# Performance work log

Measured on AMD Instinct MI355X. Metric: run time of the kernel, lower is better.

## Reference

```python
import jax, jax.numpy as jnp
import numpy as np

B, T, D = 2, 2048, 1024
H = 4            # num_heads (== num_kv_heads, num_kv_groups = 1)
W = 512          # window_size
S = 64           # state_size
CK = D // H      # head_k_dim = 256
CV = D // H      # head_v_dim = 256
EPS = 1e-5
SCALE = 1.0


def setup_inputs() -> dict:
    key = jax.random.key(0)
    ks = jax.random.split(key, 8)
    def w(k, o, i):
        return jax.random.normal(k, (o, i), jnp.float32) * 0.02
    return {
        "hidden_states": jax.random.normal(ks[0], (B, T, D), jnp.float32),
        "w_norm": jnp.ones((D,), jnp.float32),   # shared RMSNorm weight (pre- and post-norm; module overwrites self.norm)
        "Wq": w(ks[1], D, D),
        "Wk": w(ks[2], D, D),
        "Wv": w(ks[3], D, D),
        "Ws": w(ks[4], D, D),
        "Wg": w(ks[5], H * S, D),
        "Wo": w(ks[6], D, D),
    }


def _rms(x, w):
    return x * jax.lax.rsqrt(jnp.mean(x * x, axis=-1, keepdims=True) + EPS) * w


def reference(hidden_states, w_norm, Wq, Wk, Wv, Ws, Wg, Wo):
    h = _rms(hidden_states, w_norm)                           # pre-norm (norm_first)
    proj = lambda x, Wm: jnp.einsum('btd,od->bto', x, Wm)
    heads = lambda x, c: x.reshape(B, T, H, c).transpose(0, 2, 1, 3)
    q = heads(proj(h, Wq), CK) * SCALE                        # [B,H,T,CK]
    k = heads(proj(h, Wk), CK)
    v = heads(proj(h, Wv), CV)
    s = heads(proj(h, Ws), CK)                                # state-key projection
    g = jax.nn.softmax(proj(h, Wg), axis=-1)                  # softmax over full H*S dim (as in module)
    g = heads(g, S)                                           # [B,H,T,S] gate over state slots

    # ---- compressed global state (causal cumulative g-weighted outer products) ----
    # state_K[t] = sum_{t'<=t} g[t']^T s[t'];  scores_state[t,s] = q[t] . state_K[t,s]
    causal = jnp.tril(jnp.ones((T, T), dtype=bool))
    A = jnp.einsum('bhtc,bhuc->bhtu', q, s)                   # q . s per pair
    A = jnp.where(causal, A, 0.0)
    sc_state = jnp.einsum('bhtu,bhus->bhts', A, g)            # [B,H,T,S]

    # ---- sliding-window local attention (blocked: each query block sees prev+cur key block) ----
    nb = T // W
    qb = q.reshape(B, H, nb, W, CK)
    kb = k.reshape(B, H, nb, W, CK)
    vb = v.reshape(B, H, nb, W, CV)
    kprev = jnp.concatenate([jnp.zeros_like(kb[:, :, :1]), kb[:, :, :-1]], axis=2)
    vprev = jnp.concatenate([jnp.zeros_like(vb[:, :, :1]), vb[:, :, :-1]], axis=2)
    k2 = jnp.concatenate([kprev, kb], axis=3)                 # [B,H,nb,2W,CK]
    v2 = jnp.concatenate([vprev, vb], axis=3)                 # [B,H,nb,2W,CV]
    sc_w = jnp.einsum('bhnrc,bhnuc->bhnru', qb, k2)           # [B,H,nb,W,2W]

    r = jnp.arange(W)[:, None]
    u = jnp.arange(2 * W)[None, :]
    d = W + r - u                                             # distance t - t_key
    band = (d >= 0) & (d <= W - 1)                            # window of size W, causal
    first_blk = band & (u >= W)                               # block 0 has no real prev block
    wmask = jnp.where(jnp.arange(nb)[:, None, None] == 0, first_blk, band)   # [nb,W,2W]
    slopes = 2.0 ** (-8.0 * jnp.arange(H, dtype=jnp.float32) / H)            # [H]
    bias = -slopes[:, None, None] * d                          # alibi: slopes*(j-W+1) == -slope*dist
    sc_w = sc_w + bias[None, :, None, :, :]
    sc_w = jnp.where(wmask[None, None], sc_w, -1e30)

    # ---- joint softmax over [state ; window] columns ----
    sc = jnp.concatenate([sc_state.reshape(B, H, nb, W, S), sc_w], axis=-1)  # [B,H,nb,W,S+2W]
    p = jax.nn.softmax(sc, axis=-1)
    p_state = p[..., :S].reshape(B, H, T, S)
    p_w = p[..., S:]

    o_w = jnp.einsum('bhnru,bhnuc->bhnrc', p_w, v2).reshape(B, H, T, CV)
    # out_state[t] = sum_s p_state[t,s] * state_V[t,s],  state_V[t] = sum_{t'<=t} g[t']^T v[t']
    M = jnp.einsum('bhts,bhus->bhtu', p_state, g)
    M = jnp.where(causal, M, 0.0)
    o_s = jnp.einsum('bhtu,bhuc->bhtc', M, v)

    o = (o_w + o_s).transpose(0, 2, 1, 3).reshape(B, T, H * CV)
    o = o * jax.nn.sigmoid(o)                                  # swish
    o = _rms(o, w_norm)                                        # rms_norm_linear
    return jnp.einsum('btd,od->bto', o, Wo)
```

## Files before the change

### kernel.cpp

```cpp
#include <hip/hip_runtime.h>
#include <stdint.h>

#define B_  2
#define T_  2048
#define D_  1024
#define H_  4
#define S_  64
#define W_  512
#define CK_ 256
#define NC_ 32

typedef __attribute__((ext_vector_type(8))) short bf16x8;
typedef __attribute__((ext_vector_type(4))) float f32x4;
typedef __attribute__((ext_vector_type(4))) unsigned short u16x4;

__device__ __forceinline__ float bf2f(unsigned short u){ return __uint_as_float(((unsigned int)u)<<16); }
__device__ __forceinline__ unsigned short f2bf(float f){
  unsigned int u = __float_as_uint(f);
  u += 0x7fffu + ((u>>16)&1u);
  return (unsigned short)(u>>16);
}
__device__ __forceinline__ void split2(float y, unsigned short& hi, unsigned short& lo){
  hi = f2bf(y);
  lo = f2bf(y - bf2f(hi));
// ... 175 lines not shown
  __shared__ float red[256];
  red[tid]=x; __syncthreads();
  for(int s=128;s>0;s>>=1){ if(tid<s) red[tid]=fmaxf(red[tid],red[tid+s]); __syncthreads(); }
  float m = red[0]; __syncthreads();
  float e = expf(x-m);
  red[tid]=e; __syncthreads();
  for(int s=128;s>0;s>>=1){ if(tid<s) red[tid]+=red[tid+s]; __syncthreads(); }
  g[(size_t)row*256+tid] = e/red[0];
}

__global__ __launch_bounds__(256,1) void chunk_outer_mfma(
    const unsigned short* __restrict__ gthi, const unsigned short* __restrict__ gtlo,
    const unsigned short* __restrict__ s_bf, float* __restrict__ out)
{
  __shared__ unsigned short xh_lds[256*72];
  int n=blockIdx.x, h=blockIdx.y, b=blockIdx.z;
  int tid=threadIdx.x, lane=tid&63, w=tid>>6;
  int quad=lane>>4, lq=lane&15;
  int t0=n*64, bh=b*H_+h;

  const unsigned short* sb = s_bf + (size_t)(b*T_+t0)*D_ + h*CK_ + tid;
  for(int p2=0;p2<8;p2++){
    union{ unsigned short u[8]; bf16x8 v8; } r8;
    #pragma unroll
    for(int j=0;j<8;j++)
      r8.u[j] = sb[(size_t)(p2*8+j)*D_];
    *(bf16x8*)(void*)&xh_lds[tid*72 + p2*8] = r8.v8;
  }
  __syncthreads();

  size_t gtbase = ((size_t)bh*NC_ + n)*64;
  f32x4 acc[4][4];
  #pragma unroll
  for(int i=0;i<4;i++)
    #pragma unroll
    for(int j=0;j<4;j++) acc[i][j] = (f32x4){0.f,0.f,0.f,0.f};

  #pragma unroll
  for(int ks=0; ks<2; ks++){
    bf16x8 ah[4], al[4], bh4[4];
    #pragma unroll
    for(int mi=0;mi<4;mi++){
      ah[mi] = *(const bf16x8*)(const void*)(gthi + (gtbase + mi*16+lq)*64 + ks*32 + quad*8);
      al[mi] = *(const bf16x8*)(const void*)(gtlo + (gtbase + mi*16+lq)*64 + ks*32 + quad*8);
    }
    #pragma unroll
    for(int ni=0;ni<4;ni++)
      bh4[ni] = *(const bf16x8*)(const void*)&xh_lds[(w*64+ni*16+lq)*72 + ks*32 + quad*8];
    #pragma unroll
    for(int mi=0;mi<4;mi++)
      #pragma unroll
      for(int ni=0;ni<4;ni++){
        acc[mi][ni] = __builtin_amdgcn_mfma_f32_16x16x32_bf16(ah[mi], bh4[ni], acc[mi][ni], 0,0,0);
        acc[mi][ni] = __builtin_amdgcn_mfma_f32_16x16x32_bf16(al[mi], bh4[ni], acc[mi][ni], 0,0,0);
      }
  }
  size_t obase = ((size_t)bh*NC_ + n)*16384;
  #pragma unroll
  for(int mi=0;mi<4;mi++)
    #pragma unroll
    for(int ni=0;ni<4;ni++)
      #pragma unroll
      for(int i=0;i<4;i++){
        int s = mi*16 + quad*4 + i, c = w*64 + ni*16 + lq;
        out[obase + (size_t)s*256 + c] = acc[mi][ni][i];
      }
}

__global__ __launch_bounds__(256,1) void chunk_outer_vt(
    const unsigned short* __restrict__ gthi, const unsigned short* __restrict__ gtlo,
    const unsigned short* __restrict__ vt, const unsigned short* __restrict__ vtlo,
    float* __restrict__ out)
{
  int n=blockIdx.x, h=blockIdx.y, b=blockIdx.z;
  int tid=threadIdx.x, lane=tid&63, w=tid>>6;
  int quad=lane>>4, lq=lane&15;
  int t0=n*64, bh=b*H_+h;
  size_t gtbase = ((size_t)bh*NC_ + n)*64;
  f32x4 acc[4][4];
  #pragma unroll
  for(int i=0;i<4;i++)
    #pragma unroll
    for(int j=0;j<4;j++) acc[i][j] = (f32x4){0.f,0.f,0.f,0.f};

  #pragma unroll
  for(int ks=0; ks<2; ks++){
    bf16x8 ah[4], al[4];
    #pragma unroll
    for(int mi=0;mi<4;mi++){
      ah[mi] = *(const bf16x8*)(const void*)(gthi + (gtbase + mi*16+lq)*64 + ks*32 + quad*8);
      al[mi] = *(const bf16x8*)(const void*)(gtlo + (gtbase + mi*16+lq)*64 + ks*32 + quad*8);
    }
    #pragma unroll
    for(int ni=0;ni<4;ni++){
      size_t vo = ((size_t)(bh*256 + w*64 + ni*16 + lq))*T_ + t0 + ks*32 + quad*8;
      bf16x8 vh = *(const bf16x8*)(const void*)(vt + vo);
      bf16x8 vl = *(const bf16x8*)(const void*)(vtlo + vo);
      #pragma unroll
      for(int mi=0;mi<4;mi++){
        acc[mi][ni] = __builtin_amdgcn_mfma_f32_16x16x32_bf16(ah[mi], vh, acc[mi][ni], 0,0,0);
        acc[mi][ni] = __builtin_amdgcn_mfma_f32_16x16x32_bf16(al[mi], vh, acc[mi][ni], 0,0,0);
        acc[mi][ni] = __builtin_amdgcn_mfma_f32_16x16x32_bf16(ah[mi], vl, acc[mi][ni], 0,0,0);
      }
    }
  }
  size_t obase = ((size_t)bh*NC_ + n)*16384;
  #pragma unroll
  for(int mi=0;mi<4;mi++)
    #pragma unroll
    for(int ni=0;ni<4;ni++){
      int c = w*64 + ni*16 + lq, s0 = mi*16 + quad*4;
      *(f32x4*)&out[obase + (size_t)c*64 + s0] = acc[mi][ni];
    }
}

__global__ void chunk_prefix_split_kernel(const float* __restrict__ arr,
    unsigned short* __restrict__ hi, unsigned short* __restrict__ lo){
  int idx = blockIdx.x*256 + threadIdx.x;
  int bh = idx >> 14, e = idx & 16383;
  float run = 0.f;
  size_t base = (size_t)bh*NC_*16384 + e;
  for(int n=0;n<NC_;n++){
    size_t a = base + (size_t)n*16384;
    float t = arr[a];
    unsigned short hh, ll;
    split2(run, hh, ll);
    hi[a] = hh; lo[a] = ll;
    run += t;
  }
}

__global__ __launch_bounds__(256) void g_transpose_split_kernel(const float* __restrict__ g,
    unsigned short* __restrict__ gthi, unsigned short* __restrict__ gtlo){
  int n=blockIdx.x, h=blockIdx.y, b=blockIdx.z;
  int tid=threadIdx.x, t0=n*64;
  __shared__ float tt[64][65];
  #pragma unroll
  for(int p=0;p<16;p++){
    int u = (tid>>6) + p*4, s = tid&63;
    tt[s][u] = g[((size_t)(b*T_ + t0 + u))*256 + h*64 + s];
  }
  __syncthreads();
  size_t base = ((size_t)(b*H_+h)*NC_ + n)*64;
  #pragma unroll
  for(int p=0;p<16;p++){
    int s = (tid>>6) + p*4, u = tid&63;
    unsigned short hh, ll;
    split2(tt[s][u], hh, ll);
    gthi[(base+s)*64 + u] = hh;
    gtlo[(base+s)*64 + u] = ll;
  }
}

__global__ __launch_bounds__(256,1) void sc_state_mfma(
    const unsigned short* __restrict__ q_bf,
    const unsigned short* __restrict__ s_bf,
    const unsigned short* __restrict__ S1hi, const unsigned short* __restrict__ S1lo,
    const unsigned short* __restrict__ gthi, const unsigned short* __restrict__ gtlo,
    float* __restrict__ sc_state)
{
  int n=blockIdx.x, h=blockIdx.y, b=blockIdx.z;
  int tid=threadIdx.x, lane=tid&63, w=tid>>6;
  int quad=lane>>4, lq=lane&15;
  int t0=n*64, bh=b*H_+h, strip=w*16;

  __shared__ unsigned short A_hi[64*72];
  __shared__ unsigned short A_lo[64*72];

  bf16x8 qf[8];
  const unsigned short* qrow = q_bf + ((size_t)(b*T_ + t0 + strip + lq))*D_ + h*CK_ + quad*8;
  #pragma unroll
  for(int ks=0;ks<8;ks++) qf[ks] = *(const bf16x8*)(const void*)(qrow + ks*32);

  const unsigned short* sbase = s_bf + ((size_t)(b*T_ + t0))*D_ + h*CK_;
  f32x4 a1[4];
  #pragma unroll
  for(int nf=0;nf<4;nf++) a1[nf] = (f32x4){0.f,0.f,0.f,0.f};
  #pragma unroll
  for(int ks=0;ks<8;ks++){
    #pragma unroll
    for(int nf=0;nf<4;nf++){
      bf16x8 sf = *(const bf16x8*)(const void*)(sbase + (size_t)(nf*16+lq)*D_ + ks*32 + quad*8);
      a1[nf] = __builtin_amdgcn_mfma_f32_16x16x32_bf16(qf[ks], sf, a1[nf], 0,0,0);
    }
  }
  #pragma unroll
  for(int nf=0;nf<4;nf++){
    int u = nf*16 + lq;
    #pragma unroll
    for(int i=0;i<4;i++){
      int trow = strip + quad*4 + i;
      float val = (u <= trow) ? a1[nf][i] : 0.f;
      unsigned short hh, ll;
      split2(val, hh, ll);
      A_hi[trow*72 + u] = hh;
      A_lo[trow*72 + u] = ll;
    }
  }
  __syncthreads();

  bf16x8 afh[2], afl[2];
  #pragma unroll
  for(int ks=0;ks<2;ks++){
    afh[ks] = *(const bf16x8*)(const void*)&A_hi[(strip+lq)*72 + ks*32 + quad*8];
    afl[ks] = *(const bf16x8*)(const void*)&A_lo[(strip+lq)*72 + ks*32 + quad*8];
  }

  size_t s1base = ((size_t)bh*NC_ + n)*16384;
  size_t gtbase = ((size_t)bh*NC_ + n)*64;
  f32x4 acc2[4];
  #pragma unroll
  for(int nf=0;nf<4;nf++) acc2[nf] = (f32x4){0.f,0.f,0.f,0.f};
  #pragma unroll
  for(int ks=0;ks<8;ks++){
    #pragma unroll
    for(int nf=0;nf<4;nf++){
      size_t off = s1base + (size_t)(nf*16+lq)*256 + ks*32 + quad*8;
      bf16x8 b1 = *(const bf16x8*)(const void*)(S1hi + off);
      acc2[nf] = __builtin_amdgcn_mfma_f32_16x16x32_bf16(qf[ks], b1, acc2[nf], 0,0,0);
      bf16x8 b2 = *(const bf16x8*)(const void*)(S1lo + off);
      acc2[nf] = __builtin_amdgcn_mfma_f32_16x16x32_bf16(qf[ks], b2, acc2[nf], 0,0,0);
    }
  }
  #pragma unroll
  for(int ks=0;ks<2;ks++){
    #pragma unroll
    for(int nf=0;nf<4;nf++){
      size_t off = (gtbase + nf*16+lq)*64 + ks*32 + quad*8;
      bf16x8 gh = *(const bf16x8*)(const void*)(gthi + off);
      bf16x8 gl = *(const bf16x8*)(const void*)(gtlo + off);
      acc2[nf] = __builtin_amdgcn_mfma_f32_16x16x32_bf16(afh[ks], gh, acc2[nf], 0,0,0);
      acc2[nf] = __builtin_amdgcn_mfma_f32_16x16x32_bf16(afh[ks], gl, acc2[nf], 0,0,0);
      acc2[nf] = __builtin_amdgcn_mfma_f32_16x16x32_bf16(afl[ks], gh, acc2[nf], 0,0,0);
    }
  }
  #pragma unroll
  for(int nf=0;nf<4;nf++){
    #pragma unroll
    for(int i=0;i<4;i++){
      int trow = strip + quad*4 + i;
      sc_state[((size_t)bh*T_ + t0 + trow)*64 + nf*16+lq] = acc2[nf][i];
    }
  }
}

__global__ __launch_bounds__(256,1) void window_attn_mfma(
    const unsigned short* __restrict__ q_bf,
    const unsigned short* __restrict__ k_bf,
    const unsigned short* __restrict__ vt_bf,
    const float* __restrict__ sc_state,
    float* __restrict__ o,
    unsigned short* __restrict__ phi, unsigned short* __restrict__ plo)
{
  int nt=blockIdx.x, h=blockIdx.y, b=blockIdx.z;
  int tid=threadIdx.x;
  int lane = tid & 63, w = tid >> 6;
  int quad = lane >> 4, lq = lane & 15;
  int sp = w >> 1, np = w & 1;
  int t0 = nt*64, bh = b*H_ + h;
  float slope = exp2f(-2.0f*(float)h);

  __shared__ unsigned short kv_lds[256*72];
  __shared__ float S_lds[64*68];
  __shared__ unsigned short P_lds[64*72];
  __shared__ float m_lds[64], l_lds[64], al_lds[64];

  bf16x8 qf[2][8];
  #pragma unroll
  for(int st=0; st<2; st++){
    const unsigned short* qrow = q_bf + ((size_t)(b*T_ + t0 + 32*sp + 16*st + lq))*D_ + h*CK_ + quad*8;
    #pragma unroll
    for(int ks=0; ks<8; ks++)
      qf[st][ks] = *(const bf16x8*)(const void*)(qrow + ks*32);
  }

  int r = tid >> 2, part = tid & 3;
  {
    const float* scrow = sc_state + ((size_t)bh*T_ + t0 + r)*64 + part*16;
    float pm = -1e30f, sv[16];
    #pragma unroll
    for(int i=0;i<16;i++){ sv[i] = scrow[i]; pm = fmaxf(pm, sv[i]); }
    pm = fmaxf(pm, __shfl_xor(pm,1)); pm = fmaxf(pm, __shfl_xor(pm,2));
    float ps = 0.f;
    #pragma unroll
    for(int i=0;i<16;i++) ps += __expf(sv[i]-pm);
    ps += __shfl_xor(ps,1); ps += __shfl_xor(ps,2);
    if(part==0){ m_lds[r]=pm; l_lds[r]=ps; }
  }

  f32x4 o_acc[2][8];
  #pragma unroll
  for(int st=0;st<2;st++)
    #pragma unroll
    for(int nv=0;nv<8;nv++) o_acc[st][nv] = (f32x4){0.f,0.f,0.f,0.f};
  __syncthreads();

  int jt0 = (nt>=8)? nt-8 : 0;
  for(int jt=jt0; jt<=nt; jt++){
    int j0 = jt*64;
    {
      int row = tid>>2, seg = tid&3;
      const unsigned short* src = k_bf + ((size_t)(b*T_ + j0 + row))*D_ + h*CK_ + seg*64;
      unsigned short* dst = kv_lds + row*260 + seg*64;
      #pragma unroll
      for(int i=0;i<8;i++) *(bf16x8*)(void*)(dst + i*8) = *(const bf16x8*)(const void*)(src + i*8);
    }
    __syncthreads();
    f32x4 sacc[2][2];
    #pragma unroll
    for(int st=0;st<2;st++)
      #pragma unroll
      for(int n2=0;n2<2;n2++) sacc[st][n2] = (f32x4){0.f,0.f,0.f,0.f};
    #pragma unroll
    for(int n2=0;n2<2;n2++){
      int n = np*2 + n2;
      #pragma unroll
      for(int ks=0;ks<8;ks++){
        bf16x8 kf = *(const bf16x8*)(const void*)(kv_lds + (n*16+lq)*260 + ks*32 + quad*8);
        sacc[0][n2] = __builtin_amdgcn_mfma_f32_16x16x32_bf16(qf[0][ks], kf, sacc[0][n2], 0,0,0);
        sacc[1][n2] = __builtin_amdgcn_mfma_f32_16x16x32_bf16(qf[1][ks], kf, sacc[1][n2], 0,0,0);
      }
    }
    #pragma unroll
    for(int st=0;st<2;st++){
      #pragma unroll
      for(int n2=0;n2<2;n2++){
        int n = np*2+n2;
        int u = j0 + n*16 + lq;
        #pragma unroll
        for(int i=0;i<4;i++){
          int row = 32*sp + 16*st + quad*4 + i;
          int d = (t0 + row) - u;
          float val = (d>=0 && d<W_) ? sacc[st][n2][i] - slope*(float)d : -1e30f;
          S_lds[row*68 + n*16+lq] = val;
        }
      }
    }
    __syncthreads();
    {
      float s16[16], tm = -1e30f;
      #pragma unroll
      for(int i=0;i<16;i++){ s16[i] = S_lds[r*68 + part*16 + i]; tm = fmaxf(tm, s16[i]); }
      tm = fmaxf(tm, __shfl_xor(tm,1)); tm = fmaxf(tm, __shfl_xor(tm,2));
      float m_old = m_lds[r];
      float m_new = fmaxf(m_old, tm);
      float alpha = __expf(m_old - m_new);
      float ts = 0.f;
      union { unsigned short u[16]; bf16x8 v[2]; } pk;
      #pragma unroll
      for(int i=0;i<16;i++){ float p = __expf(s16[i]-m_new); ts += p; pk.u[i] = f2bf(p); }
      ts += __shfl_xor(ts,1); ts += __shfl_xor(ts,2);
      *(bf16x8*)(void*)&P_lds[r*72 + part*16]     = pk.v[0];
      *(bf16x8*)(void*)&P_lds[r*72 + part*16 + 8] = pk.v[1];
      if(part==0){ m_lds[r] = m_new; l_lds[r] = l_lds[r]*alpha + ts; al_lds[r] = alpha; }
      #pragma unroll
      for(int pass=0; pass<4; pass++){
        int cv = (tid>>2) + 64*pass, useg = (tid&3)*16;
        const unsigned short* src = vt_bf + ((size_t)(bh*256 + cv))*T_ + j0 + useg;
        unsigned short* dst = kv_lds + cv*72 + useg;
        *(bf16x8*)(void*)(dst)   = *(const bf16x8*)(const void*)(src);
        *(bf16x8*)(void*)(dst+8) = *(const bf16x8*)(const void*)(src+8);
      }
    }
    __syncthreads();
    #pragma unroll
    for(int st=0;st<2;st++){
      #pragma unroll
      for(int i=0;i<4;i++){
        float al = al_lds[32*sp+16*st+quad*4+i];
        #pragma unroll
        for(int nv=0;nv<8;nv++) o_acc[st][nv][i] *= al;
      }
    }
    bf16x8 pa[2][2];
    #pragma unroll
    for(int st=0;st<2;st++)
      #pragma unroll
      for(int k2=0;k2<2;k2++)
        pa[st][k2] = *(const bf16x8*)(const void*)&P_lds[(32*sp+16*st+lq)*72 + k2*32 + quad*8];
    #pragma unroll
    for(int nv=0;nv<8;nv++){
      int cvt = np*8 + nv;
      #pragma unroll
      for(int k2=0;k2<2;k2++){
        bf16x8 vb = *(const bf16x8*)(const void*)(kv_lds + (cvt*16+lq)*72 + k2*32 + quad*8);
        o_acc[0][nv] = __builtin_amdgcn_mfma_f32_16x16x32_bf16(pa[0][k2], vb, o_acc[0][nv], 0,0,0);
        o_acc[1][nv] = __builtin_amdgcn_mfma_f32_16x16x32_bf16(pa[1][k2], vb, o_acc[1][nv], 0,0,0);
      }
    }
    __syncthreads();
  }
  #pragma unroll
  for(int st=0;st<2;st++){
    #pragma unroll
    for(int i=0;i<4;i++){
      int row = 32*sp+16*st+quad*4+i;
      float rl = 1.0f / l_lds[row];
      #pragma unroll
      for(int nv=0;nv<8;nv++){
        int cv = (np*8+nv)*16 + lq;
        o[((size_t)bh*T_ + t0 + row)*256 + cv] = o_acc[st][nv][i] * rl;
      }
    }
  }
  {
    float mf = m_lds[r], rlf = 1.0f / l_lds[r];
    const float* scrow = sc_state + ((size_t)bh*T_ + t0 + r)*64 + part*16;
    size_t pb = ((size_t)bh*T_ + t0 + r)*64 + part*16;
    #pragma unroll
    for(int i=0;i<16;i++){
      float pv = __expf(scrow[i]-mf)*rlf;
      unsigned short hh, ll;
      split2(pv, hh, ll);
      phi[pb+i] = hh;
      plo[pb+i] = ll;
    }
  }
}

__global__ __launch_bounds__(256,1) void o_state_mfma(
    const unsigned short* __restrict__ phi, const unsigned short* __restrict__ plo,
    const float* __restrict__ g,
    const unsigned short* __restrict__ S2hi, const unsigned short* __restrict__ S2lo,
    const unsigned short* __restrict__ vt, const unsigned short* __restrict__ vtlo,
    float* __restrict__ o)
{
  __shared__ unsigned short gh_lds[64*72];
  __shared__ unsigned short gl_lds[64*72];
  __shared__ unsigned short Mh_lds[64*72];
  __shared__ unsigned short Ml_lds[64*72];
  int n=blockIdx.x, h=blockIdx.y, b=blockIdx.z;
  int tid=threadIdx.x, lane=tid&63, w=tid>>6;
  int quad=lane>>4, lq=lane&15;
  int t0=n*64, bh=b*H_+h, strip=w*16;

  {
    int gu = tid>>2, gs0 = (tid&3)*16;
    const float* gr = g + ((size_t)(b*T_+t0+gu))*256 + h*64 + gs0;
    union{ unsigned short u[16]; bf16x8 v[2]; } GH, GL;
    #pragma unroll
    for(int j=0;j<16;j++) split2(gr[j], GH.u[j], GL.u[j]);
    *(bf16x8*)(void*)&gh_lds[gu*72+gs0]   = GH.v[0];
    *(bf16x8*)(void*)&gh_lds[gu*72+gs0+8] = GH.v[1];
    *(bf16x8*)(void*)&gl_lds[gu*72+gs0]   = GL.v[0];
    *(bf16x8*)(void*)&gl_lds[gu*72+gs0+8] = GL.v[1];
  }
  __syncthreads();

  {
    const unsigned short* ph = phi + ((size_t)bh*T_ + t0 + strip + lq)*64;
    const unsigned short* pl = plo + ((size_t)bh*T_ + t0 + strip + lq)*64;
    f32x4 ma[4];
    #pragma unroll
    for(int nf=0;nf<4;nf++) ma[nf] = (f32x4){0.f,0.f,0.f,0.f};
    #pragma unroll
    for(int ks=0;ks<2;ks++){
      bf16x8 pfh = *(const bf16x8*)(const void*)(ph + ks*32 + quad*8);
      bf16x8 pfl = *(const bf16x8*)(const void*)(pl + ks*32 + quad*8);
      #pragma unroll
      for(int nf=0;nf<4;nf++){
        bf16x8 gH = *(const bf16x8*)(const void*)&gh_lds[(nf*16+lq)*72 + ks*32 + quad*8];
        bf16x8 gL = *(const bf16x8*)(const void*)&gl_lds[(nf*16+lq)*72 + ks*32 + quad*8];
        ma[nf] = __builtin_amdgcn_mfma_f32_16x16x32_bf16(pfh, gH, ma[nf], 0,0,0);
        ma[nf] = __builtin_amdgcn_mfma_f32_16x16x32_bf16(pfh, gL, ma[nf], 0,0,0);
        ma[nf] = __builtin_amdgcn_mfma_f32_16x16x32_bf16(pfl, gH, ma[nf], 0,0,0);
      }
    }
    #pragma unroll
    for(int nf=0;nf<4;nf++){
      int u = nf*16 + lq;
      #pragma unroll
      for(int i=0;i<4;i++){
        int trow = strip + quad*4 + i;
        float val = (u <= trow) ? ma[nf][i] : 0.f;
        unsigned short hh, ll;
        split2(val, hh, ll);
        Mh_lds[trow*72 + u] = hh;
        Ml_lds[trow*72 + u] = ll;
      }
    }
  }
  __syncthreads();

  f32x4 oacc[4][4];
  #pragma unroll
  for(int i=0;i<4;i++)
    #pragma unroll
    for(int j=0;j<4;j++) oacc[i][j] = (f32x4){0.f,0.f,0.f,0.f};
  int c0 = w*64;
  size_t sgbase = ((size_t)bh*NC_ + n)*16384;
  #pragma unroll
  for(int ks=0;ks<2;ks++){
    bf16x8 pAh[4], pAl[4], mAh[4], mAl[4];
    #pragma unroll
    for(int mi=0;mi<4;mi++){
      size_t po = ((size_t)bh*T_ + t0 + mi*16+lq)*64 + ks*32 + quad*8;
      pAh[mi] = *(const bf16x8*)(const void*)(phi + po);
      pAl[mi] = *(const bf16x8*)(const void*)(plo + po);
      mAh[mi] = *(const bf16x8*)(const void*)&Mh_lds[(mi*16+lq)*72 + ks*32 + quad*8];
      mAl[mi] = *(const bf16x8*)(const void*)&Ml_lds[(mi*16+lq)*72 + ks*32 + quad*8];
    }
    #pragma unroll
    for(int ni=0;ni<4;ni++){
      int c = c0 + ni*16 + lq;
      size_t so = sgbase + (size_t)c*64 + ks*32 + quad*8;
      bf16x8 sgH = *(const bf16x8*)(const void*)(S2hi + so);
      bf16x8 sgL = *(const bf16x8*)(const void*)(S2lo + so);
      size_t vo = ((size_t)(bh*256 + c))*T_ + t0 + ks*32 + quad*8;
      bf16x8 vH = *(const bf16x8*)(const void*)(vt + vo);
      bf16x8 vL = *(const bf16x8*)(const void*)(vtlo + vo);
      #pragma unroll
      for(int mi=0;mi<4;mi++){
        oacc[mi][ni] = __builtin_amdgcn_mfma_f32_16x16x32_bf16(pAh[mi], sgH, oacc[mi][ni], 0,0,0);
        oacc[mi][ni] = __builtin_amdgcn_mfma_f32_16x16x32_bf16(pAh[mi], sgL, oacc[mi][ni], 0,0,0);
        oacc[mi][ni] = __builtin_amdgcn_mfma_f32_16x16x32_bf16(pAl[mi], sgH, oacc[mi][ni], 0,0,0);
        oacc[mi][ni] = __builtin_amdgcn_mfma_f32_16x16x32_bf16(mAh[mi], vH, oacc[mi][ni], 0,0,0);
        oacc[mi][ni] = __builtin_amdgcn_mfma_f32_16x16x32_bf16(mAl[mi], vH, oacc[mi][ni], 0,0,0);
        oacc[mi][ni] = __builtin_amdgcn_mfma_f32_16x16x32_bf16(mAh[mi], vL, oacc[mi][ni], 0,0,0);
      }
    }
  }
  #pragma unroll
  for(int mi=0;mi<4;mi++)
    #pragma unroll
    for(int ni=0;ni<4;ni++)
      #pragma unroll
      for(int i=0;i<4;i++){
        int trow = mi*16 + quad*4 + i, c = c0 + ni*16 + lq;
        size_t oi = ((size_t)bh*T_ + t0 + trow)*256 + c;
        o[oi] += oacc[mi][ni][i];
      }
}

__global__ void swish_rms_split_kernel(const float* __restrict__ o, const float* __restrict__ w,
                                       unsigned short* __restrict__ ohi, unsigned short* __restrict__ olo){
  int bt=blockIdx.x, tid=threadIdx.x;
  int b = bt >> 11, t = bt & 2047;
  float y[4]; float ss=0.f;
  #pragma unroll
  for(int hh=0;hh<4;hh++){
    float x = o[((size_t)(b*H_+hh)*T_ + t)*256 + tid];
    float yy = x / (1.f + expf(-x));
    y[hh]=yy; ss += yy*yy;
  }
  __shared__ float red[256];
  red[tid]=ss; __syncthreads();
  for(int s2=128;s2>0;s2>>=1){ if(tid<s2) red[tid]+=red[tid+s2]; __syncthreads(); }
  float r = rsqrtf(red[0]/1024.f + 1e-5f);
  #pragma unroll
  for(int hh=0;hh<4;hh++){
    unsigned short a,bq;
    split2(y[hh]*r*w[hh*256+tid], a, bq);
    ohi[(size_t)bt*1024 + hh*256 + tid] = a;
    olo[(size_t)bt*1024 + hh*256 + tid] = bq;
  }
}

extern "C" void kernel_launch(void* const* d_in, const int* in_sizes, int n_in,
                              void* d_out, int out_size, void* d_ws, size_t ws_size,
                              hipStream_t stream){
  const float* hidden = (const float*)d_in[0];
  const float* w_norm = (const float*)d_in[1];
  const float* Wq = (const float*)d_in[2];
  const float* Wk = (const float*)d_in[3];
  const float* Wv = (const float*)d_in[4];
  const float* Ws = (const float*)d_in[5];
  const float* Wg = (const float*)d_in[6];
  const float* Wo = (const float*)d_in[7];
  float* out = (float*)d_out;

  char* p = (char*)d_ws;
  auto alloc = [&](size_t bytes)->void*{ void* r = (void*)p; p += (bytes + 255) & ~(size_t)255; return r; };
  unsigned short* h_hi = (unsigned short*)alloc(8388608);
  unsigned short* h_lo = (unsigned short*)alloc(8388608);
  unsigned short* Wc_hi = (unsigned short*)alloc(11010048);
  unsigned short* Wc_lo = (unsigned short*)alloc(11010048);
  unsigned short* vslot = (unsigned short*)alloc(16777216);
  float* g   = (float*)alloc(4194304);
  float* P1  = (float*)alloc(16777216);
  float* P2  = (float*)alloc(16777216);
  float* sc  = (float*)alloc(4194304);
  float* ps  = (float*)alloc(4194304);
  unsigned short* qks = (unsigned short*)alloc(25165824);
  unsigned short* vt  = (unsigned short*)alloc(8388608);

  unsigned short* vtlo = vslot;
  unsigned short* S2hi = vslot + 4194304;
  unsigned short* q_bf = qks;
  unsigned short* k_bf = qks + 4194304;
  unsigned short* s_bf = qks + 8388608;
  unsigned short* S2lo = s_bf;
  float* o = P1;
  unsigned short* S1hi = (unsigned short*)P2;
  unsigned short* S1lo = S1hi + 4194304;
  unsigned short* GThi = (unsigned short*)ps;
  unsigned short* GTlo = GThi + 1048576;
  unsigned short* phi  = (unsigned short*)ps;
  unsigned short* plo  = phi + 1048576;

  rmsnorm_split_kernel<<<4096,256,0,stream>>>(hidden, w_norm, h_hi, h_lo);
  wsplit_kernel<<<5376,256,0,stream>>>(Wq, Wk, Ws, Wv, Wg, Wo, Wc_hi, Wc_lo);
  gemm_bf16s<<<dim3(34,32),256,0,stream>>>(h_hi, h_lo, Wc_hi, Wc_lo,
                                           qks, vt, vtlo, g, nullptr, 0);
  softmax256_kernel<<<4096,256,0,stream>>>(g);
  dim3 gc(32,4,2);
  g_transpose_split_kernel<<<gc,256,0,stream>>>(g, GThi, GTlo);
  chunk_outer_mfma<<<gc,256,0,stream>>>(GThi, GTlo, s_bf, P1);
  chunk_prefix_split_kernel<<<512,256,0,stream>>>(P1, S1hi, S1lo);
  sc_state_mfma<<<gc,256,0,stream>>>(q_bf, s_bf, S1hi, S1lo, GThi, GTlo, sc);
  chunk_outer_vt<<<gc,256,0,stream>>>(GThi, GTlo, vt, vtlo, P2);
  chunk_prefix_split_kernel<<<512,256,0,stream>>>(P2, S2hi, S2lo);
  window_attn_mfma<<<gc,256,0,stream>>>(q_bf, k_bf, vt, sc, o, phi, plo);
  o_state_mfma<<<gc,256,0,stream>>>(phi, plo, g, S2hi, S2lo, vt, vtlo, o);
  swish_rms_split_kernel<<<4096,256,0,stream>>>(o, w_norm, h_hi, h_lo);
  gemm_bf16s<<<dim3(8,32),256,0,stream>>>(h_hi, h_lo, Wc_hi + (size_t)4352*1024, Wc_lo + (size_t)4352*1024,
                                          nullptr, nullptr, nullptr, nullptr, out, 1);
}
```

Baseline: 385.5 us.

## Split sc_state and window attention blocks into 32-row halves for more parallelism

Both sc_state_mfma and window_attn_mfma now launch twice as many blocks, each handling 32 query rows instead of 64, with launch bounds raised to allow two blocks per CU. The original grid of 256 blocks underfills a 256-CU MI355X, so the change aims to raise occupancy and latency hiding. In exchange, K/V tiles and S1/G operands are loaded once per half-block, which doubles that global and LDS traffic per query row, and the per-row softmax reductions are regrouped to 8 threads per row.

```diff
diff --git a/kernel.cpp b/kernel.cpp
--- a/kernel.cpp
+++ b/kernel.cpp
@@ -351,49 +351,53 @@
   }
 }
 
-__global__ __launch_bounds__(256,1) void sc_state_mfma(
+__global__ __launch_bounds__(256,2) void sc_state_mfma(
     const unsigned short* __restrict__ q_bf,
     const unsigned short* __restrict__ s_bf,
     const unsigned short* __restrict__ S1hi, const unsigned short* __restrict__ S1lo,
     const unsigned short* __restrict__ gthi, const unsigned short* __restrict__ gtlo,
     float* __restrict__ sc_state)
 {
-  int n=blockIdx.x, h=blockIdx.y, b=blockIdx.z;
+  int bx=blockIdx.x, h=blockIdx.y, b=blockIdx.z;
+  int nt=bx>>1, half=bx&1;
   int tid=threadIdx.x, lane=tid&63, w=tid>>6;
   int quad=lane>>4, lq=lane&15;
-  int t0=n*64, bh=b*H_+h, strip=w*16;
-
-  __shared__ unsigned short A_hi[64*72];
-  __shared__ unsigned short A_lo[64*72];
+  int t0c=nt*64, t0h=t0c+half*32, bh=b*H_+h;
+  int strip16=(w&1)*16, nsel=w>>1;
+
+  __shared__ unsigned short A_hi[32*72];
+  __shared__ unsigned short A_lo[32*72];
 
   bf16x8 qf[8];
-  const unsigned short* qrow = q_bf + ((size_t)(b*T_ + t0 + strip + lq))*D_ + h*CK_ + quad*8;
+  const unsigned short* qrow = q_bf + ((size_t)(b*T_ + t0h + strip16 + lq))*D_ + h*CK_ + quad*8;
   #pragma unroll
   for(int ks=0;ks<8;ks++) qf[ks] = *(const bf16x8*)(const void*)(qrow + ks*32);
 
-  const unsigned short* sbase = s_bf + ((size_t)(b*T_ + t0))*D_ + h*CK_;
-  f32x4 a1[4];
-  #pragma unroll
-  for(int nf=0;nf<4;nf++) a1[nf] = (f32x4){0.f,0.f,0.f,0.f};
+  const unsigned short* sbase = s_bf + ((size_t)(b*T_ + t0c))*D_ + h*CK_;
+  f32x4 a1[2];
+  #pragma unroll
+  for(int nf2=0;nf2<2;nf2++) a1[nf2] = (f32x4){0.f,0.f,0.f,0.f};
   #pragma unroll
   for(int ks=0;ks<8;ks++){
     #pragma unroll
-    for(int nf=0;nf<4;nf++){
+    for(int nf2=0;nf2<2;nf2++){
+      int nf = nsel*2 + nf2;
       bf16x8 sf = *(const bf16x8*)(const void*)(sbase + (size_t)(nf*16+lq)*D_ + ks*32 + quad*8);
-      a1[nf] = __builtin_amdgcn_mfma_f32_16x16x32_bf16(qf[ks], sf, a1[nf], 0,0,0);
-    }
-  }
-  #pragma unroll
-  for(int nf=0;nf<4;nf++){
-    int u = nf*16 + lq;
+      a1[nf2] = __builtin_amdgcn_mfma_f32_16x16x32_bf16(qf[ks], sf, a1[nf2], 0,0,0);
+    }
+  }
+  #pragma unroll
+  for(int nf2=0;nf2<2;nf2++){
+    int u = (nsel*2+nf2)*16 + lq;
     #pragma unroll
     for(int i=0;i<4;i++){
-      int trow = strip + quad*4 + i;
-      float val = (u <= trow) ? a1[nf][i] : 0.f;
+      int lr = strip16 + quad*4 + i;
+      int trow = half*32 + lr;
+      float val = (u <= trow) ? a1[nf2][i] : 0.f;
       unsigned short hh, ll;
       split2(val, hh, ll);
-      A_hi[trow*72 + u] = hh;
-      A_lo[trow*72 + u] = ll;
+      A_hi[lr*72 + u] = hh;
+      A_lo[lr*72 + u] = ll;
     }
   }
   __syncthreads();
@@ -401,49 +405,52 @@
   bf16x8 afh[2], afl[2];
   #pragma unroll
   for(int ks=0;ks<2;ks++){
-    afh[ks] = *(const bf16x8*)(const void*)&A_hi[(strip+lq)*72 + ks*32 + quad*8];
-    afl[ks] = *(const bf16x8*)(const void*)&A_lo[(strip+lq)*72 + ks*32 + quad*8];
-  }
-
-  size_t s1base = ((size_t)bh*NC_ + n)*16384;
-  size_t gtbase = ((size_t)bh*NC_ + n)*64;
-  f32x4 acc2[4];
-  #pragma unroll
-  for(int nf=0;nf<4;nf++) acc2[nf] = (f32x4){0.f,0.f,0.f,0.f};
+    afh[ks] = *(const bf16x8*)(const void*)&A_hi[(strip16+lq)*72 + ks*32 + quad*8];
+    afl[ks] = *(const bf16x8*)(const void*)&A_lo[(strip16+lq)*72 + ks*32 + quad*8];
+  }
+
+  size_t s1base = ((size_t)bh*NC_ + nt)*16384;
+  size_t gtbase = ((size_t)bh*NC_ + nt)*64;
+  f32x4 acc2[2];
+  #pragma unroll
+  for(int nf2=0;nf2<2;nf2++) acc2[nf2] = (f32x4){0.f,0.f,0.f,0.f};
   #pragma unroll
   for(int ks=0;ks<8;ks++){
     #pragma unroll
-    for(int nf=0;nf<4;nf++){
+    for(int nf2=0;nf2<2;nf2++){
+      int nf = nsel*2 + nf2;
       size_t off = s1base + (size_t)(nf*16+lq)*256 + ks*32 + quad*8;
       bf16x8 b1 = *(const bf16x8*)(const void*)(S1hi + off);
-      acc2[nf] = __builtin_amdgcn_mfma_f32_16x16x32_bf16(qf[ks], b1, acc2[nf], 0,0,0);
+      acc2[nf2] = __builtin_amdgcn_mfma_f32_16x16x32_bf16(qf[ks], b1, acc2[nf2], 0,0,0);
       bf16x8 b2 = *(const bf16x8*)(const void*)(S1lo + off);
-      acc2[nf] = __builtin_amdgcn_mfma_f32_16x16x32_bf16(qf[ks], b2, acc2[nf], 0,0,0);
+      acc2[nf2] = __builtin_amdgcn_mfma_f32_16x16x32_bf16(qf[ks], b2, acc2[nf2], 0,0,0);
     }
   }
   #pragma unroll
   for(int ks=0;ks<2;ks++){
     #pragma unroll
-    for(int nf=0;nf<4;nf++){
+    for(int nf2=0;nf2<2;nf2++){
+      int nf = nsel*2 + nf2;
       size_t off = (gtbase + nf*16+lq)*64 + ks*32 + quad*8;
       bf16x8 gh = *(const bf16x8*)(const void*)(gthi + off);
       bf16x8 gl = *(const bf16x8*)(const void*)(gtlo + off);
-      acc2[nf] = __builtin_amdgcn_mfma_f32_16x16x32_bf16(afh[ks], gh, acc2[nf], 0,0,0);
-      acc2[nf] = __builtin_amdgcn_mfma_f32_16x16x32_bf16(afh[ks], gl, acc2[nf], 0,0,0);
-      acc2[nf] = __builtin_amdgcn_mfma_f32_16x16x32_bf16(afl[ks], gh, acc2[nf], 0,0,0);
-    }
-  }
-  #pragma unroll
-  for(int nf=0;nf<4;nf++){
+      acc2[nf2] = __builtin_amdgcn_mfma_f32_16x16x32_bf16(afh[ks], gh, acc2[nf2], 0,0,0);
+      acc2[nf2] = __builtin_amdgcn_mfma_f32_16x16x32_bf16(afh[ks], gl, acc2[nf2], 0,0,0);
+      acc2[nf2] = __builtin_amdgcn_mfma_f32_16x16x32_bf16(afl[ks], gh, acc2[nf2], 0,0,0);
+    }
+  }
+  #pragma unroll
+  for(int nf2=0;nf2<2;nf2++){
+    int nf = nsel*2 + nf2;
     #pragma unroll
     for(int i=0;i<4;i++){
-      int trow = strip + quad*4 + i;
-      sc_state[((size_t)bh*T_ + t0 + trow)*64 + nf*16+lq] = acc2[nf][i];
-    }
-  }
-}
-
-__global__ __launch_bounds__(256,1) void window_attn_mfma(
+      int lr = strip16 + quad*4 + i;
+      sc_state[((size_t)bh*T_ + t0h + lr)*64 + nf*16+lq] = acc2[nf2][i];
+    }
+  }
+}
+
+__global__ __launch_bounds__(256,2) void window_attn_mfma(
     const unsigned short* __restrict__ q_bf,
     const unsigned short* __restrict__ k_bf,
     const unsigned short* __restrict__ vt_bf,
@@ -451,47 +458,45 @@
     float* __restrict__ o,
     unsigned short* __restrict__ phi, unsigned short* __restrict__ plo)
 {
-  int nt=blockIdx.x, h=blockIdx.y, b=blockIdx.z;
+  int bx=blockIdx.x, h=blockIdx.y, b=blockIdx.z;
+  int nt = bx>>1, half = bx&1;
   int tid=threadIdx.x;
   int lane = tid & 63, w = tid >> 6;
   int quad = lane >> 4, lq = lane & 15;
   int sp = w >> 1, np = w & 1;
-  int t0 = nt*64, bh = b*H_ + h;
+  int t0c = nt*64, t0h = t0c + half*32, bh = b*H_ + h;
   float slope = exp2f(-2.0f*(float)h);
 
   __shared__ unsigned short kv_lds[256*72];
-  __shared__ float S_lds[64*68];
-  __shared__ unsigned short P_lds[64*72];
-  __shared__ float m_lds[64], l_lds[64], al_lds[64];
-
-  bf16x8 qf[2][8];
-  #pragma unroll
-  for(int st=0; st<2; st++){
-    const unsigned short* qrow = q_bf + ((size_t)(b*T_ + t0 + 32*sp + 16*st + lq))*D_ + h*CK_ + quad*8;
+  __shared__ float S_lds[32*68];
+  __shared__ unsigned short P_lds[32*72];
+  __shared__ float m_lds[32], l_lds[32], al_lds[32];
+
+  bf16x8 qf[8];
+  {
+    const unsigned short* qrow = q_bf + ((size_t)(b*T_ + t0h + 16*sp + lq))*D_ + h*CK_ + quad*8;
     #pragma unroll
     for(int ks=0; ks<8; ks++)
-      qf[st][ks] = *(const bf16x8*)(const void*)(qrow + ks*32);
-  }
-
-  int r = tid >> 2, part = tid & 3;
+      qf[ks] = *(const bf16x8*)(const void*)(qrow + ks*32);
+  }
+
+  int r = tid >> 3, part = tid & 7;
   {
-    const float* scrow = sc_state + ((size_t)bh*T_ + t0 + r)*64 + part*16;
-    float pm = -1e30f, sv[16];
-    #pragma unroll
-    for(int i=0;i<16;i++){ sv[i] = scrow[i]; pm = fmaxf(pm, sv[i]); }
-    pm = fmaxf(pm, __shfl_xor(pm,1)); pm = fmaxf(pm, __shfl_xor(pm,2));
+    const float* scrow = sc_state + ((size_t)bh*T_ + t0h + r)*64 + part*8;
+    float pm = -1e30f, sv[8];
+    #pragma unroll
+    for(int i=0;i<8;i++){ sv[i] = scrow[i]; pm = fmaxf(pm, sv[i]); }
+    pm = fmaxf(pm, __shfl_xor(pm,1)); pm = fmaxf(pm, __shfl_xor(pm,2)); pm = fmaxf(pm, __shfl_xor(pm,4));
     float ps = 0.f;
     #pragma unroll
-    for(int i=0;i<16;i++) ps += __expf(sv[i]-pm);
-    ps += __shfl_xor(ps,1); ps += __shfl_xor(ps,2);
+    for(int i=0;i<8;i++) ps += __expf(sv[i]-pm);
+    ps += __shfl_xor(ps,1); ps += __shfl_xor(ps,2); ps += __shfl_xor(ps,4);
     if(part==0){ m_lds[r]=pm; l_lds[r]=ps; }
   }
 
-  f32x4 o_acc[2][8];
-  #pragma unroll
-  for(int st=0;st<2;st++)
-    #pragma unroll
-    for(int nv=0;nv<8;nv++) o_acc[st][nv] = (f32x4){0.f,0.f,0.f,0.f};
+  f32x4 o_acc[8];
+  #pragma unroll
+  for(int nv=0;nv<8;nv++) o_acc[nv] = (f32x4){0.f,0.f,0.f,0.f};
   __syncthreads();
 
   int jt0 = (nt>=8)? nt-8 : 0;
@@ -505,52 +510,45 @@
       for(int i=0;i<8;i++) *(bf16x8*)(void*)(dst + i*8) = *(const bf16x8*)(const void*)(src + i*8);
     }
     __syncthreads();
-    f32x4 sacc[2][2];
-    #pragma unroll
-    for(int st=0;st<2;st++)
-      #pragma unroll
-      for(int n2=0;n2<2;n2++) sacc[st][n2] = (f32x4){0.f,0.f,0.f,0.f};
+    f32x4 sacc[2];
+    #pragma unroll
+    for(int n2=0;n2<2;n2++) sacc[n2] = (f32x4){0.f,0.f,0.f,0.f};
     #pragma unroll
     for(int n2=0;n2<2;n2++){
       int n = np*2 + n2;
       #pragma unroll
       for(int ks=0;ks<8;ks++){
         bf16x8 kf = *(const bf16x8*)(const void*)(kv_lds + (n*16+lq)*260 + ks*32 + quad*8);
-        sacc[0][n2] = __builtin_amdgcn_mfma_f32_16x16x32_bf16(qf[0][ks], kf, sacc[0][n2], 0,0,0);
-        sacc[1][n2] = __builtin_amdgcn_mfma_f32_16x16x32_bf16(qf[1][ks], kf, sacc[1][n2], 0,0,0);
-      }
-    }
-    #pragma unroll
-    for(int st=0;st<2;st++){
-      #pragma unroll
-      for(int n2=0;n2<2;n2++){
-        int n = np*2+n2;
-        int u = j0 + n*16 + lq;
-        #pragma unroll
-        for(int i=0;i<4;i++){
-          int row = 32*sp + 16*st + quad*4 + i;
-          int d = (t0 + row) - u;
-          float val = (d>=0 && d<W_) ? sacc[st][n2][i] - slope*(float)d : -1e30f;
-          S_lds[row*68 + n*16+lq] = val;
-        }
+        sacc[n2] = __builtin_amdgcn_mfma_f32_16x16x32_bf16(qf[ks], kf, sacc[n2], 0,0,0);
+      }
+    }
+    #pragma unroll
+    for(int n2=0;n2<2;n2++){
+      int n = np*2+n2;
+      int u = j0 + n*16 + lq;
+      #pragma unroll
+      for(int i=0;i<4;i++){
+        int row = 16*sp + quad*4 + i;
+        int d = (t0h + row) - u;
+        float val = (d>=0 && d<W_) ? sacc[n2][i] - slope*(float)d : -1e30f;
+        S_lds[row*68 + n*16+lq] = val;
       }
     }
     __syncthreads();
     {
-      float s16[16], tm = -1e30f;
-      #pragma unroll
-      for(int i=0;i<16;i++){ s16[i] = S_lds[r*68 + part*16 + i]; tm = fmaxf(tm, s16[i]); }
-      tm = fmaxf(tm, __shfl_xor(tm,1)); tm = fmaxf(tm, __shfl_xor(tm,2));
+      float s8[8], tm = -1e30f;
+      #pragma unroll
+      for(int i=0;i<8;i++){ s8[i] = S_lds[r*68 + part*8 + i]; tm = fmaxf(tm, s8[i]); }
+      tm = fmaxf(tm, __shfl_xor(tm,1)); tm = fmaxf(tm, __shfl_xor(tm,2)); tm = fmaxf(tm, __shfl_xor(tm,4));
       float m_old = m_lds[r];
       float m_new = fmaxf(m_old, tm);
       float alpha = __expf(m_old - m_new);
       float ts = 0.f;
-      union { unsigned short u[16]; bf16x8 v[2]; } pk;
-      #pragma unroll
-      for(int i=0;i<16;i++){ float p = __expf(s16[i]-m_new); ts += p; pk.u[i] = f2bf(p); }
-      ts += __shfl_xor(ts,1); ts += __shfl_xor(ts,2);
-      *(bf16x8*)(void*)&P_lds[r*72 + part*16]     = pk.v[0];
-      *(bf16x8*)(void*)&P_lds[r*72 + part*16 + 8] = pk.v[1];
+      union { unsigned short u[8]; bf16x8 v; } pk;
+      #pragma unroll
+      for(int i=0;i<8;i++){ float p = __expf(s8[i]-m_new); ts += p; pk.u[i] = f2bf(p); }
+      ts += __shfl_xor(ts,1); ts += __shfl_xor(ts,2); ts += __shfl_xor(ts,4);
+      *(bf16x8*)(void*)&P_lds[r*72 + part*8] = pk.v;
       if(part==0){ m_lds[r] = m_new; l_lds[r] = l_lds[r]*alpha + ts; al_lds[r] = alpha; }
       #pragma unroll
       for(int pass=0; pass<4; pass++){
@@ -563,51 +561,42 @@
     }
     __syncthreads();
     #pragma unroll
-    for(int st=0;st<2;st++){
-      #pragma unroll
-      for(int i=0;i<4;i++){
-        float al = al_lds[32*sp+16*st+quad*4+i];
-        #pragma unroll
-        for(int nv=0;nv<8;nv++) o_acc[st][nv][i] *= al;
-      }
-    }
-    bf16x8 pa[2][2];
-    #pragma unroll
-    for(int st=0;st<2;st++)
-      #pragma unroll
-      for(int k2=0;k2<2;k2++)
-        pa[st][k2] = *(const bf16x8*)(const void*)&P_lds[(32*sp+16*st+lq)*72 + k2*32 + quad*8];
+    for(int i=0;i<4;i++){
+      float al = al_lds[16*sp+quad*4+i];
+      #pragma unroll
+      for(int nv=0;nv<8;nv++) o_acc[nv][i] *= al;
+    }
+    bf16x8 pa[2];
+    #pragma unroll
+    for(int k2=0;k2<2;k2++)
+      pa[k2] = *(const bf16x8*)(const void*)&P_lds[(16*sp+lq)*72 + k2*32 + quad*8];
     #pragma unroll
     for(int nv=0;nv<8;nv++){
       int cvt = np*8 + nv;
       #pragma unroll
       for(int k2=0;k2<2;k2++){
         bf16x8 vb = *(const bf16x8*)(const void*)(kv_lds + (cvt*16+lq)*72 + k2*32 + quad*8);
-        o_acc[0][nv] = __builtin_amdgcn_mfma_f32_16x16x32_bf16(pa[0][k2], vb, o_acc[0][nv], 0,0,0);
-        o_acc[1][nv] = __builtin_amdgcn_mfma_f32_16x16x32_bf16(pa[1][k2], vb, o_acc[1][nv], 0,0,0);
+        o_acc[nv] = __builtin_amdgcn_mfma_f32_16x16x32_bf16(pa[k2], vb, o_acc[nv], 0,0,0);
       }
     }
     __syncthreads();
   }
   #pragma unroll
-  for(int st=0;st<2;st++){
-    #pragma unroll
-    for(int i=0;i<4;i++){
-      int row = 32*sp+16*st+quad*4+i;
-      float rl = 1.0f / l_lds[row];
-      #pragma unroll
-      for(int nv=0;nv<8;nv++){
-        int cv = (np*8+nv)*16 + lq;
-        o[((size_t)bh*T_ + t0 + row)*256 + cv] = o_acc[st][nv][i] * rl;
-      }
+  for(int i=0;i<4;i++){
+    int row = 16*sp + quad*4 + i;
+    float rl = 1.0f / l_lds[row];
+    #pragma unroll
+    for(int nv=0;nv<8;nv++){
+      int cv = (np*8+nv)*16 + lq;
+      o[((size_t)bh*T_ + t0h + row)*256 + cv] = o_acc[nv][i] * rl;
     }
   }
   {
     float mf = m_lds[r], rlf = 1.0f / l_lds[r];
-    const float* scrow = sc_state + ((size_t)bh*T_ + t0 + r)*64 + part*16;
-    size_t pb = ((size_t)bh*T_ + t0 + r)*64 + part*16;
-    #pragma unroll
-    for(int i=0;i<16;i++){
+    const float* scrow = sc_state + ((size_t)bh*T_ + t0h + r)*64 + part*8;
+    size_t pb = ((size_t)bh*T_ + t0h + r)*64 + part*8;
+    #pragma unroll
+    for(int i=0;i<8;i++){
       float pv = __expf(scrow[i]-mf)*rlf;
       unsigned short hh, ll;
       split2(pv, hh, ll);
@@ -803,13 +792,14 @@
                                            qks, vt, vtlo, g, nullptr, 0);
   softmax256_kernel<<<4096,256,0,stream>>>(g);
   dim3 gc(32,4,2);
+  dim3 gch(64,4,2);
   g_transpose_split_kernel<<<gc,256,0,stream>>>(g, GThi, GTlo);
   chunk_outer_mfma<<<gc,256,0,stream>>>(GThi, GTlo, s_bf, P1);
   chunk_prefix_split_kernel<<<512,256,0,stream>>>(P1, S1hi, S1lo);
-  sc_state_mfma<<<gc,256,0,stream>>>(q_bf, s_bf, S1hi, S1lo, GThi, GTlo, sc);
+  sc_state_mfma<<<gch,256,0,stream>>>(q_bf, s_bf, S1hi, S1lo, GThi, GTlo, sc);
   chunk_outer_vt<<<gc,256,0,stream>>>(GThi, GTlo, vt, vtlo, P2);
   chunk_prefix_split_kernel<<<512,256,0,stream>>>(P2, S2hi, S2lo);
-  window_attn_mfma<<<gc,256,0,stream>>>(q_bf, k_bf, vt, sc, o, phi, plo);
+  window_attn_mfma<<<gch,256,0,stream>>>(q_bf, k_bf, vt, sc, o, phi, plo);
   o_state_mfma<<<gc,256,0,stream>>>(phi, plo, g, S2hi, S2lo, vt, vtlo, o);
   swish_rms_split_kernel<<<4096,256,0,stream>>>(o, w_norm, h_hi, h_lo);
   gemm_bf16s<<<dim3(8,32),256,0,stream>>>(h_hi, h_lo, Wc_hi + (size_t)4352*1024, Wc_lo + (size_t)4352*1024,
```

Result: slower. 402.5 us (+4.4%).

## Split window attention work across 8 waves per block instead of 4

Applied to the files above, without the earlier changes.

Raises the window-attention block from 256 to 512 threads so each of the 8 waves owns one 16-row query strip instead of two. Per-thread register state (Q fragments, accumulators) halves, and the softmax rows, K and V tile loads are spread over twice as many threads. This adds more waves per block to hide latency, at the cost of more per-thread barrier overhead and duplicated K/V fragment reads from LDS.

```diff
diff --git a/kernel.cpp b/kernel.cpp
--- a/kernel.cpp
+++ b/kernel.cpp
@@ -443,7 +443,7 @@
   }
 }
 
-__global__ __launch_bounds__(256,1) void window_attn_mfma(
+__global__ __launch_bounds__(512,1) void window_attn_mfma(
     const unsigned short* __restrict__ q_bf,
     const unsigned short* __restrict__ k_bf,
     const unsigned short* __restrict__ vt_bf,
@@ -464,97 +464,87 @@
   __shared__ unsigned short P_lds[64*72];
   __shared__ float m_lds[64], l_lds[64], al_lds[64];
 
-  bf16x8 qf[2][8];
-  #pragma unroll
-  for(int st=0; st<2; st++){
-    const unsigned short* qrow = q_bf + ((size_t)(b*T_ + t0 + 32*sp + 16*st + lq))*D_ + h*CK_ + quad*8;
+  bf16x8 qf[8];
+  {
+    const unsigned short* qrow = q_bf + ((size_t)(b*T_ + t0 + 16*sp + lq))*D_ + h*CK_ + quad*8;
     #pragma unroll
     for(int ks=0; ks<8; ks++)
-      qf[st][ks] = *(const bf16x8*)(const void*)(qrow + ks*32);
-  }
-
-  int r = tid >> 2, part = tid & 3;
+      qf[ks] = *(const bf16x8*)(const void*)(qrow + ks*32);
+  }
+
+  int r = tid >> 3, part = tid & 7;
   {
-    const float* scrow = sc_state + ((size_t)bh*T_ + t0 + r)*64 + part*16;
-    float pm = -1e30f, sv[16];
-    #pragma unroll
-    for(int i=0;i<16;i++){ sv[i] = scrow[i]; pm = fmaxf(pm, sv[i]); }
-    pm = fmaxf(pm, __shfl_xor(pm,1)); pm = fmaxf(pm, __shfl_xor(pm,2));
+    const float* scrow = sc_state + ((size_t)bh*T_ + t0 + r)*64 + part*8;
+    float pm = -1e30f, sv[8];
+    #pragma unroll
+    for(int i=0;i<8;i++){ sv[i] = scrow[i]; pm = fmaxf(pm, sv[i]); }
+    pm = fmaxf(pm, __shfl_xor(pm,1)); pm = fmaxf(pm, __shfl_xor(pm,2)); pm = fmaxf(pm, __shfl_xor(pm,4));
     float ps = 0.f;
     #pragma unroll
-    for(int i=0;i<16;i++) ps += __expf(sv[i]-pm);
-    ps += __shfl_xor(ps,1); ps += __shfl_xor(ps,2);
+    for(int i=0;i<8;i++) ps += __expf(sv[i]-pm);
+    ps += __shfl_xor(ps,1); ps += __shfl_xor(ps,2); ps += __shfl_xor(ps,4);
     if(part==0){ m_lds[r]=pm; l_lds[r]=ps; }
   }
 
-  f32x4 o_acc[2][8];
-  #pragma unroll
-  for(int st=0;st<2;st++)
-    #pragma unroll
-    for(int nv=0;nv<8;nv++) o_acc[st][nv] = (f32x4){0.f,0.f,0.f,0.f};
+  f32x4 o_acc[8];
+  #pragma unroll
+  for(int nv=0;nv<8;nv++) o_acc[nv] = (f32x4){0.f,0.f,0.f,0.f};
   __syncthreads();
 
   int jt0 = (nt>=8)? nt-8 : 0;
   for(int jt=jt0; jt<=nt; jt++){
     int j0 = jt*64;
     {
-      int row = tid>>2, seg = tid&3;
-      const unsigned short* src = k_bf + ((size_t)(b*T_ + j0 + row))*D_ + h*CK_ + seg*64;
-      unsigned short* dst = kv_lds + row*260 + seg*64;
-      #pragma unroll
-      for(int i=0;i<8;i++) *(bf16x8*)(void*)(dst + i*8) = *(const bf16x8*)(const void*)(src + i*8);
+      int row = tid>>3, seg = tid&7;
+      const unsigned short* src = k_bf + ((size_t)(b*T_ + j0 + row))*D_ + h*CK_ + seg*32;
+      unsigned short* dst = kv_lds + row*260 + seg*32;
+      #pragma unroll
+      for(int i=0;i<4;i++) *(bf16x8*)(void*)(dst + i*8) = *(const bf16x8*)(const void*)(src + i*8);
     }
     __syncthreads();
-    f32x4 sacc[2][2];
-    #pragma unroll
-    for(int st=0;st<2;st++)
-      #pragma unroll
-      for(int n2=0;n2<2;n2++) sacc[st][n2] = (f32x4){0.f,0.f,0.f,0.f};
+    f32x4 sacc[2];
+    #pragma unroll
+    for(int n2=0;n2<2;n2++) sacc[n2] = (f32x4){0.f,0.f,0.f,0.f};
     #pragma unroll
     for(int n2=0;n2<2;n2++){
       int n = np*2 + n2;
       #pragma unroll
       for(int ks=0;ks<8;ks++){
         bf16x8 kf = *(const bf16x8*)(const void*)(kv_lds + (n*16+lq)*260 + ks*32 + quad*8);
-        sacc[0][n2] = __builtin_amdgcn_mfma_f32_16x16x32_bf16(qf[0][ks], kf, sacc[0][n2], 0,0,0);
-        sacc[1][n2] = __builtin_amdgcn_mfma_f32_16x16x32_bf16(qf[1][ks], kf, sacc[1][n2], 0,0,0);
-      }
-    }
-    #pragma unroll
-    for(int st=0;st<2;st++){
-      #pragma unroll
-      for(int n2=0;n2<2;n2++){
-        int n = np*2+n2;
-        int u = j0 + n*16 + lq;
-        #pragma unroll
-        for(int i=0;i<4;i++){
-          int row = 32*sp + 16*st + quad*4 + i;
-          int d = (t0 + row) - u;
-          float val = (d>=0 && d<W_) ? sacc[st][n2][i] - slope*(float)d : -1e30f;
-          S_lds[row*68 + n*16+lq] = val;
-        }
+        sacc[n2] = __builtin_amdgcn_mfma_f32_16x16x32_bf16(qf[ks], kf, sacc[n2], 0,0,0);
+      }
+    }
+    #pragma unroll
+    for(int n2=0;n2<2;n2++){
+      int n = np*2+n2;
+      int u = j0 + n*16 + lq;
+      #pragma unroll
+      for(int i=0;i<4;i++){
+        int row = 16*sp + quad*4 + i;
+        int d = (t0 + row) - u;
+        float val = (d>=0 && d<W_) ? sacc[n2][i] - slope*(float)d : -1e30f;
+        S_lds[row*68 + n*16+lq] = val;
       }
     }
     __syncthreads();
     {
-      float s16[16], tm = -1e30f;
-      #pragma unroll
-      for(int i=0;i<16;i++){ s16[i] = S_lds[r*68 + part*16 + i]; tm = fmaxf(tm, s16[i]); }
-      tm = fmaxf(tm, __shfl_xor(tm,1)); tm = fmaxf(tm, __shfl_xor(tm,2));
+      float s8[8], tm = -1e30f;
+      #pragma unroll
+      for(int i=0;i<8;i++){ s8[i] = S_lds[r*68 + part*8 + i]; tm = fmaxf(tm, s8[i]); }
+      tm = fmaxf(tm, __shfl_xor(tm,1)); tm = fmaxf(tm, __shfl_xor(tm,2)); tm = fmaxf(tm, __shfl_xor(tm,4));
       float m_old = m_lds[r];
       float m_new = fmaxf(m_old, tm);
       float alpha = __expf(m_old - m_new);
       float ts = 0.f;
-      union { unsigned short u[16]; bf16x8 v[2]; } pk;
-      #pragma unroll
-      for(int i=0;i<16;i++){ float p = __expf(s16[i]-m_new); ts += p; pk.u[i] = f2bf(p); }
-      ts += __shfl_xor(ts,1); ts += __shfl_xor(ts,2);
-      *(bf16x8*)(void*)&P_lds[r*72 + part*16]     = pk.v[0];
-      *(bf16x8*)(void*)&P_lds[r*72 + part*16 + 8] = pk.v[1];
+      union { unsigned short u[8]; bf16x8 v; } pk;
+      #pragma unroll
+      for(int i=0;i<8;i++){ float p = __expf(s8[i]-m_new); ts += p; pk.u[i] = f2bf(p); }
+      ts += __shfl_xor(ts,1); ts += __shfl_xor(ts,2); ts += __shfl_xor(ts,4);
+      *(bf16x8*)(void*)&P_lds[r*72 + part*8] = pk.v;
       if(part==0){ m_lds[r] = m_new; l_lds[r] = l_lds[r]*alpha + ts; al_lds[r] = alpha; }
       #pragma unroll
-      for(int pass=0; pass<4; pass++){
-        int cv = (tid>>2) + 64*pass, useg = (tid&3)*16;
+      for(int pass=0; pass<2; pass++){
+        int cv = (tid>>2) + 128*pass, useg = (tid&3)*16;
         const unsigned short* src = vt_bf + ((size_t)(bh*256 + cv))*T_ + j0 + useg;
         unsigned short* dst = kv_lds + cv*72 + useg;
         *(bf16x8*)(void*)(dst)   = *(const bf16x8*)(const void*)(src);
@@ -563,51 +553,42 @@
     }
     __syncthreads();
     #pragma unroll
-    for(int st=0;st<2;st++){
-      #pragma unroll
-      for(int i=0;i<4;i++){
-        float al = al_lds[32*sp+16*st+quad*4+i];
-        #pragma unroll
-        for(int nv=0;nv<8;nv++) o_acc[st][nv][i] *= al;
-      }
-    }
-    bf16x8 pa[2][2];
-    #pragma unroll
-    for(int st=0;st<2;st++)
-      #pragma unroll
-      for(int k2=0;k2<2;k2++)
-        pa[st][k2] = *(const bf16x8*)(const void*)&P_lds[(32*sp+16*st+lq)*72 + k2*32 + quad*8];
+    for(int i=0;i<4;i++){
+      float al = al_lds[16*sp+quad*4+i];
+      #pragma unroll
+      for(int nv=0;nv<8;nv++) o_acc[nv][i] *= al;
+    }
+    bf16x8 pa[2];
+    #pragma unroll
+    for(int k2=0;k2<2;k2++)
+      pa[k2] = *(const bf16x8*)(const void*)&P_lds[(16*sp+lq)*72 + k2*32 + quad*8];
     #pragma unroll
     for(int nv=0;nv<8;nv++){
       int cvt = np*8 + nv;
       #pragma unroll
       for(int k2=0;k2<2;k2++){
         bf16x8 vb = *(const bf16x8*)(const void*)(kv_lds + (cvt*16+lq)*72 + k2*32 + quad*8);
-        o_acc[0][nv] = __builtin_amdgcn_mfma_f32_16x16x32_bf16(pa[0][k2], vb, o_acc[0][nv], 0,0,0);
-        o_acc[1][nv] = __builtin_amdgcn_mfma_f32_16x16x32_bf16(pa[1][k2], vb, o_acc[1][nv], 0,0,0);
+        o_acc[nv] = __builtin_amdgcn_mfma_f32_16x16x32_bf16(pa[k2], vb, o_acc[nv], 0,0,0);
       }
     }
     __syncthreads();
   }
   #pragma unroll
-  for(int st=0;st<2;st++){
-    #pragma unroll
-    for(int i=0;i<4;i++){
-      int row = 32*sp+16*st+quad*4+i;
-      float rl = 1.0f / l_lds[row];
-      #pragma unroll
-      for(int nv=0;nv<8;nv++){
-        int cv = (np*8+nv)*16 + lq;
-        o[((size_t)bh*T_ + t0 + row)*256 + cv] = o_acc[st][nv][i] * rl;
-      }
+  for(int i=0;i<4;i++){
+    int row = 16*sp + quad*4 + i;
+    float rl = 1.0f / l_lds[row];
+    #pragma unroll
+    for(int nv=0;nv<8;nv++){
+      int cv = (np*8+nv)*16 + lq;
+      o[((size_t)bh*T_ + t0 + row)*256 + cv] = o_acc[nv][i] * rl;
     }
   }
   {
     float mf = m_lds[r], rlf = 1.0f / l_lds[r];
-    const float* scrow = sc_state + ((size_t)bh*T_ + t0 + r)*64 + part*16;
-    size_t pb = ((size_t)bh*T_ + t0 + r)*64 + part*16;
-    #pragma unroll
-    for(int i=0;i<16;i++){
+    const float* scrow = sc_state + ((size_t)bh*T_ + t0 + r)*64 + part*8;
+    size_t pb = ((size_t)bh*T_ + t0 + r)*64 + part*8;
+    #pragma unroll
+    for(int i=0;i<8;i++){
       float pv = __expf(scrow[i]-mf)*rlf;
       unsigned short hh, ll;
       split2(pv, hh, ll);
@@ -809,7 +790,7 @@
   sc_state_mfma<<<gc,256,0,stream>>>(q_bf, s_bf, S1hi, S1lo, GThi, GTlo, sc);
   chunk_outer_vt<<<gc,256,0,stream>>>(GThi, GTlo, vt, vtlo, P2);
   chunk_prefix_split_kernel<<<512,256,0,stream>>>(P2, S2hi, S2lo);
-  window_attn_mfma<<<gc,256,0,stream>>>(q_bf, k_bf, vt, sc, o, phi, plo);
+  window_attn_mfma<<<gc,512,0,stream>>>(q_bf, k_bf, vt, sc, o, phi, plo);
   o_state_mfma<<<gc,256,0,stream>>>(phi, plo, g, S2hi, S2lo, vt, vtlo, o);
   swish_rms_split_kernel<<<4096,256,0,stream>>>(o, w_norm, h_hi, h_lo);
   gemm_bf16s<<<dim3(8,32),256,0,stream>>>(h_hi, h_lo, Wc_hi + (size_t)4352*1024, Wc_lo + (size_t)4352*1024,
```

After: 391.6 us. No clear change (+1.6%).
